# Performance work log

Hardware: AMD Instinct MI355X
Metric: run time of the kernel (lower is better)

Reference implementation:

```python
import jax, jax.numpy as jnp
import numpy as np

D_MODEL = 1024
N_HEADS = 16
D_FF = 4096
LN_EPS = 1e-5


def _layernorm(x, g, b):
    mu = jnp.mean(x, axis=-1, keepdims=True)
    var = jnp.var(x, axis=-1, keepdims=True)
    return (x - mu) * jax.lax.rsqrt(var + LN_EPS) * g + b


def setup_inputs() -> dict:
    key = jax.random.key(0)
    ks = jax.random.split(key, 10)
    N, B, C, F = 2048, 4, D_MODEL, D_FF
    s = lambda fan_in: 1.0 / np.sqrt(fan_in)
    return {
        "src": jax.random.normal(ks[0], (N, B, C), dtype=jnp.float32),
        "ln_g": jnp.ones((C,), jnp.float32),
        "ln_b": jnp.zeros((C,), jnp.float32),
        "w_qkv": jax.random.normal(ks[1], (C, 3 * C), jnp.float32) * s(C),
        "w_proj": jax.random.normal(ks[2], (C, C), jnp.float32) * s(C),
        "b_proj": jnp.zeros((C,), jnp.float32),
        "w1": jax.random.normal(ks[3], (C, F), jnp.float32) * s(C),
        "b1": jnp.zeros((F,), jnp.float32),
        "w2": jax.random.normal(ks[4], (F, C), jnp.float32) * s(F),
        "b2": jnp.zeros((C,), jnp.float32),
    }


def reference(src, ln_g, ln_b, w_qkv, w_proj, b_proj, w1, b1, w2, b2):
    N, B, C = src.shape
    H = N_HEADS
    hd = C // H
    scale = hd ** -0.5

    # pre-norm (norm_first=True)
    x = _layernorm(src, ln_g, ln_b)

    # qkv: (N,B,3C) -> (N,B,3,H,hd) -> permute(2,1,3,0,4) = (3,B,H,N,hd)
    qkv = (x @ w_qkv).reshape(N, B, 3, H, hd).transpose(2, 1, 3, 0, 4)
    q, k, v = qkv[0], qkv[1], qkv[2]  # (B,H,N,hd)

    attn = jax.nn.softmax(jnp.einsum("bhnd,bhmd->bhnm", q, k) * scale, axis=-1)
    o = jnp.einsum("bhnm,bhmd->bhnd", attn, v)  # (B,H,N,hd)
    # faithful to original: transpose(0,2) -> (N,H,B,hd), then reshape (N,B,C)
    o = o.transpose(2, 1, 0, 3).reshape(N, B, C)
    o = o @ w_proj + b_proj

    src = src + o
    # post_norm is Identity (norm_first=True)
    h = jax.nn.gelu(src @ w1 + b1, approximate=False)
    src = src + (h @ w2 + b2)
    return src
```

## Files before the change

### kernel.cpp

```cpp
#include <hip/hip_runtime.h>
#include <math.h>

typedef unsigned short u16;
typedef __attribute__((ext_vector_type(4))) unsigned short u16x4;
typedef __attribute__((ext_vector_type(8))) short short8;
typedef __attribute__((ext_vector_type(4))) float f32x4;

__device__ __forceinline__ void gl_lds16(const void* g, void* s) {
  __builtin_amdgcn_global_load_lds((const __attribute__((address_space(1))) void*)g,
                                   (__attribute__((address_space(3))) void*)s, 16, 0, 0);
}

__device__ __forceinline__ u16 f2bf(float f) {
  union { float f; unsigned u; } a; a.f = f;
  unsigned r = a.u + 0x7fff + ((a.u >> 16) & 1);
  return (u16)(r >> 16);
}

__global__ __launch_bounds__(256) void ln_kernel(const float* __restrict__ src,
                                                 const float* __restrict__ g,
                                                 const float* __restrict__ b,
                                                 u16* __restrict__ out) {
  int row = blockIdx.x;
  int t = threadIdx.x;
  const float4* s4 = (const float4*)(src + (size_t)row * 1024);
  float4 x = s4[t];
  float s1 = x.x + x.y + x.z + x.w;
  float s2 = x.x * x.x + x.y * x.y + x.z * x.z + x.w * x.w;
  for (int m = 32; m; m >>= 1) { s1 += __shfl_xor(s1, m); s2 += __shfl_xor(s2, m); }
  __shared__ float red[8];
  int w = t >> 6, lane = t & 63;
  if (lane == 0) { red[w] = s1; red[4 + w] = s2; }
  __syncthreads();
  float tot  = red[0] + red[1] + red[2] + red[3];
  float tot2 = red[4] + red[5] + red[6] + red[7];
  float mean = tot * (1.0f / 1024.0f);
  float var  = tot2 * (1.0f / 1024.0f) - mean * mean;
  float rs = rsqrtf(var + 1e-5f);
  float4 gg = ((const float4*)g)[t];
  float4 bb = ((const float4*)b)[t];
  u16x4 o;
  o[0] = f2bf((x.x - mean) * rs * gg.x + bb.x);
  o[1] = f2bf((x.y - mean) * rs * gg.y + bb.y);
  o[2] = f2bf((x.z - mean) * rs * gg.z + bb.z);
  o[3] = f2bf((x.w - mean) * rs * gg.w + bb.w);
  ((u16x4*)(out + (size_t)row * 1024))[t] = o;
}

__global__ __launch_bounds__(256) void tcast_kernel(const float* __restrict__ in,
                                                    u16* __restrict__ out, int K, int N) {
  __shared__ float tt[64][65];
  int t = threadIdx.x;
  int n0 = blockIdx.x * 64, k0 = blockIdx.y * 64;
  #pragma unroll
  for (int s = 0; s < 4; ++s) {
    int idx = s * 256 + t;
    int r = idx >> 4, c4 = idx & 15;
    float4 v = *(const float4*)(in + (size_t)(k0 + r) * N + n0 + c4 * 4);
    tt[r][c4 * 4 + 0] = v.x; tt[r][c4 * 4 + 1] = v.y;
    tt[r][c4 * 4 + 2] = v.z; tt[r][c4 * 4 + 3] = v.w;
  }
  __syncthreads();
  #pragma unroll
  for (int s = 0; s < 4; ++s) {
    int idx = s * 256 + t;
    int nr = idx >> 4, kc = idx & 15;
    u16x4 o;
    o[0] = f2bf(tt[kc * 4 + 0][nr]);
    o[1] = f2bf(tt[kc * 4 + 1][nr]);
    o[2] = f2bf(tt[kc * 4 + 2][nr]);
    o[3] = f2bf(tt[kc * 4 + 3][nr]);
    *(u16x4*)(out + (size_t)(n0 + nr) * K + k0 + kc * 4) = o;
  }
}

template <int EPI>
__global__ __launch_bounds__(256, 2) void gemm_kernel(
    const u16* __restrict__ A, const u16* __restrict__ Bt,
    int M, int N, int K,
    const float* __restrict__ bias, const float* __restrict__ resid,
    float* __restrict__ outf, u16* __restrict__ outh,
    u16* __restrict__ qo, u16* __restrict__ ko, u16* __restrict__ vo) {
  __shared__ u16 lA[128 * 32];
  __shared__ u16 lB[128 * 32];
  int t = threadIdx.x, w = t >> 6, lane = t & 63;
  int bm = blockIdx.x, bn = blockIdx.y;
  int wm = (w >> 1) * 64, wn = (w & 1) * 64;
  int am = lane & 15, ag = lane >> 4;
  f32x4 acc[4][4];
  #pragma unroll
  for (int i = 0; i < 4; ++i)
    #pragma unroll
    for (int j = 0; j < 4; ++j)
      #pragma unroll
      for (int r = 0; r < 4; ++r) acc[i][j][r] = 0.f;

  const size_t rowA0 = (size_t)bm * 128, colB0 = (size_t)bn * 128;

  for (int k0 = 0; k0 < K; k0 += 32) {
    #pragma unroll
    for (int s = 0; s < 2; ++s) {
      int c = s * 256 + w * 64 + lane;
      int row = c >> 2, cc = c & 3;
      int scc = cc ^ ((row >> 1) & 3);
      gl_lds16(A  + (rowA0 + row) * K + k0 + scc * 8, (char*)lA + (size_t)(s * 256 + w * 64) * 16);
      gl_lds16(Bt + (colB0 + row) * K + k0 + scc * 8, (char*)lB + (size_t)(s * 256 + w * 64) * 16);
    }
    __syncthreads();
    short8 af[4], bfr[4];
    #pragma unroll
    for (int i = 0; i < 4; ++i) {
      int row = wm + i * 16 + am;
      int ch = ag ^ ((row >> 1) & 3);
      af[i] = *(const short8*)(lA + row * 32 + ch * 8);
    }
    #pragma unroll
    for (int j = 0; j < 4; ++j) {
      int row = wn + j * 16 + am;
      int ch = ag ^ ((row >> 1) & 3);
      bfr[j] = *(const short8*)(lB + row * 32 + ch * 8);
    }
    #pragma unroll
    for (int i = 0; i < 4; ++i)
      #pragma unroll
      for (int j = 0; j < 4; ++j)
        acc[i][j] = __builtin_amdgcn_mfma_f32_16x16x32_bf16(af[i], bfr[j], acc[i][j], 0, 0, 0);
    __syncthreads();
  }

  #pragma unroll
  for (int i = 0; i < 4; ++i) {
    #pragma unroll
    for (int j = 0; j < 4; ++j) {
      #pragma unroll
      for (int r = 0; r < 4; ++r) {
        int grow = (int)rowA0 + wm + i * 16 + ag * 4 + r;
        int gcol = (int)colB0 + wn + j * 16 + am;
        float v = acc[i][j][r];
        if (EPI == 0) {
          int which = gcol >> 10, hh = (gcol >> 6) & 15, d = gcol & 63;
          int n = grow >> 2, bb = grow & 3;
          size_t hoff = (size_t)(bb * 16 + hh);
          if (which == 0)      qo[(hoff * 2048 + n) * 64 + d] = f2bf(v);
          else if (which == 1) ko[(hoff * 2048 + n) * 64 + d] = f2bf(v);
          else                 vo[hoff * 64 * 2048 + (size_t)d * 2048 + n] = f2bf(v);
        } else if (EPI == 1) {
          size_t idx = (size_t)grow * 1024 + gcol;
          float y = resid[idx] + v + bias[gcol];
          outf[idx] = y;
          outh[idx] = f2bf(y);
        } else if (EPI == 2) {
          float x = v + bias[gcol];
          float ge = 0.5f * x * (1.0f + erff(x * 0.70710678118654752f));
          outh[(size_t)grow * 4096 + gcol] = f2bf(ge);
        } else {
          size_t idx = (size_t)grow * 1024 + gcol;
          outf[idx] = resid[idx] + v + bias[gcol];
        }
      }
    }
  }
}

__global__ __launch_bounds__(256, 2) void attn_kernel(const u16* __restrict__ Q,
                                                      const u16* __restrict__ Kt,
                                                      const u16* __restrict__ Vt,
                                                      u16* __restrict__ Omix) {
  __shared__ u16 Qs[64 * 64], Ks[64 * 64], Vs[64 * 64];
  __shared__ u16 Ps[4][16 * 72];
  int t = threadIdx.x, w = t >> 6, lane = t & 63;
  int qb = blockIdx.x, bh = blockIdx.y;
  int bb = bh >> 4, hh = bh & 15;
  const u16* qbase = Q  + ((size_t)bh * 2048 + (size_t)qb * 64) * 64;
  const u16* kbase = Kt + (size_t)bh * 2048 * 64;
  const u16* vbase = Vt + (size_t)bh * 64 * 2048;
  int am = lane & 15, ag = lane >> 4;

  #pragma unroll
  for (int s = 0; s < 2; ++s) {
    int c = (w * 2 + s) * 64 + lane;
    int row = c >> 3, cc = c & 7;
    int scc = cc ^ (row & 7);
    gl_lds16(qbase + row * 64 + scc * 8, (char*)Qs + (size_t)(w * 2 + s) * 64 * 16);
  }
  __syncthreads();
  short8 qf[2];
  #pragma unroll
  for (int hf = 0; hf < 2; ++hf) {
    int row = w * 16 + am;
    int ch = (hf * 4 + ag) ^ (row & 7);
    qf[hf] = *(const short8*)(Qs + row * 64 + ch * 8);
  }

  float m[4], l[4];
  f32x4 o[4];
  #pragma unroll
  for (int r = 0; r < 4; ++r) { m[r] = -3.0e38f; l[r] = 0.f; }
  #pragma unroll
  for (int j = 0; j < 4; ++j)
    #pragma unroll
    for (int r = 0; r < 4; ++r) o[j][r] = 0.f;

  for (int kt = 0; kt < 32; ++kt) {
    int n0 = kt * 64;
    #pragma unroll
    for (int s = 0; s < 2; ++s) {
      int c = (w * 2 + s) * 64 + lane;
      int row = c >> 3, cc = c & 7;
      int scc = cc ^ (row & 7);
      gl_lds16(kbase + (size_t)(n0 + row) * 64 + scc * 8, (char*)Ks + (size_t)(w * 2 + s) * 64 * 16);
      gl_lds16(vbase + (size_t)row * 2048 + n0 + scc * 8, (char*)Vs + (size_t)(w * 2 + s) * 64 * 16);
    }
    __syncthreads();

    f32x4 sacc[4];
    #pragma unroll
    for (int jf = 0; jf < 4; ++jf)
      #pragma unroll
      for (int r = 0; r < 4; ++r) sacc[jf][r] = 0.f;
    #pragma unroll
    for (int jf = 0; jf < 4; ++jf) {
      #pragma unroll
      for (int hf = 0; hf < 2; ++hf) {
        int row = jf * 16 + am;
        int ch = (hf * 4 + ag) ^ (row & 7);
        short8 kf = *(const short8*)(Ks + row * 64 + ch * 8);
        sacc[jf] = __builtin_amdgcn_mfma_f32_16x16x32_bf16(qf[hf], kf, sacc[jf], 0, 0, 0);
      }
    }

    float pv[4][4], alpha[4];
    #pragma unroll
    for (int r = 0; r < 4; ++r) {
      float mx = fmaxf(fmaxf(sacc[0][r], sacc[1][r]), fmaxf(sacc[2][r], sacc[3][r])) * 0.125f;
      for (int msk = 1; msk < 16; msk <<= 1) mx = fmaxf(mx, __shfl_xor(mx, msk));
      float mnew = fmaxf(m[r], mx);
      alpha[r] = __expf(m[r] - mnew);
      float rs = 0.f;
      #pragma unroll
      for (int jf = 0; jf < 4; ++jf) {
        float p = __expf(sacc[jf][r] * 0.125f - mnew);
        pv[jf][r] = p;
        rs += p;
      }
      for (int msk = 1; msk < 16; msk <<= 1) rs += __shfl_xor(rs, msk);
      l[r] = l[r] * alpha[r] + rs;
      m[r] = mnew;
    }
    #pragma unroll
    for (int jf = 0; jf < 4; ++jf)
      #pragma unroll
      for (int r = 0; r < 4; ++r) o[jf][r] *= alpha[r];

    u16* pw = Ps[w];
    #pragma unroll
    for (int jf = 0; jf < 4; ++jf)
      #pragma unroll
      for (int r = 0; r < 4; ++r)
        pw[(ag * 4 + r) * 72 + jf * 16 + am] = f2bf(pv[jf][r]);

    short8 pf[2];
    #pragma unroll
    for (int kc = 0; kc < 2; ++kc)
      pf[kc] = *(const short8*)(pw + am * 72 + kc * 32 + ag * 8);

    #pragma unroll
    for (int jf = 0; jf < 4; ++jf) {
      #pragma unroll
      for (int kc = 0; kc < 2; ++kc) {
        int row = jf * 16 + am;
        int ch = (kc * 4 + ag) ^ (row & 7);
        short8 vf = *(const short8*)(Vs + row * 64 + ch * 8);
        o[jf] = __builtin_amdgcn_mfma_f32_16x16x32_bf16(pf[kc], vf, o[jf], 0, 0, 0);
      }
    }
    __syncthreads();
  }

  #pragma unroll
  for (int jf = 0; jf < 4; ++jf) {
    #pragma unroll
    for (int r = 0; r < 4; ++r) {
      int qrow = qb * 64 + w * 16 + ag * 4 + r;
      int d = jf * 16 + am;
      float val = o[jf][r] / l[r];
      Omix[((size_t)qrow * 4 + (hh >> 2)) * 1024 + (hh & 3) * 256 + bb * 64 + d] = f2bf(val);
    }
  }
}

extern "C" void kernel_launch(void* const* d_in, const int* in_sizes, int n_in,
                              void* d_out, int out_size, void* d_ws, size_t ws_size,
                              hipStream_t stream) {
  const float* src    = (const float*)d_in[0];
  const float* ln_g   = (const float*)d_in[1];
  const float* ln_b   = (const float*)d_in[2];
  const float* w_qkv  = (const float*)d_in[3];
  const float* w_proj = (const float*)d_in[4];
  const float* b_proj = (const float*)d_in[5];
  const float* w1     = (const float*)d_in[6];
  const float* b1     = (const float*)d_in[7];
  const float* w2     = (const float*)d_in[8];
  const float* b2     = (const float*)d_in[9];

  char* ws = (char*)d_ws;
  u16* wqkvT  = (u16*)(ws + 0);
  u16* wprojT = (u16*)(ws + 6291456);
  u16* w1T    = (u16*)(ws + 8388608);
  u16* w2T    = (u16*)(ws + 16777216);
  u16* xln    = (u16*)(ws + 25165824);
  u16* Omix   = xln;
  u16* Qp     = (u16*)(ws + 41943040);
  u16* Kp     = (u16*)(ws + 58720256);
  u16* Vp     = (u16*)(ws + 75497472);
  u16* hbuf   = (u16*)(ws + 41943040);
  u16* ybf    = (u16*)(ws + 109051904);
  float* yf   = (float*)d_out;

  dim3 blk(256);
  tcast_kernel<<<dim3(48, 16), blk, 0, stream>>>(w_qkv, wqkvT, 1024, 3072);
  tcast_kernel<<<dim3(16, 16), blk, 0, stream>>>(w_proj, wprojT, 1024, 1024);
  tcast_kernel<<<dim3(64, 16), blk, 0, stream>>>(w1, w1T, 1024, 4096);
  tcast_kernel<<<dim3(16, 64), blk, 0, stream>>>(w2, w2T, 4096, 1024);
  ln_kernel<<<8192, blk, 0, stream>>>(src, ln_g, ln_b, xln);

  gemm_kernel<0><<<dim3(64, 24), blk, 0, stream>>>(xln, wqkvT, 8192, 3072, 1024,
      nullptr, nullptr, nullptr, nullptr, Qp, Kp, Vp);

  attn_kernel<<<dim3(32, 64), blk, 0, stream>>>(Qp, Kp, Vp, Omix);

  gemm_kernel<1><<<dim3(64, 8), blk, 0, stream>>>(Omix, wprojT, 8192, 1024, 1024,
      b_proj, src, yf, ybf, nullptr, nullptr, nullptr);

  gemm_kernel<2><<<dim3(64, 32), blk, 0, stream>>>(ybf, w1T, 8192, 4096, 1024,
      b1, nullptr, nullptr, hbuf, nullptr, nullptr, nullptr);

  gemm_kernel<3><<<dim3(64, 8), blk, 0, stream>>>(hbuf, w2T, 8192, 1024, 4096,
      b2, yf, (float*)d_out, nullptr, nullptr, nullptr, nullptr);
}
```

Baseline: 639.9 us.

## Rewrite attention with 32x32 MFMA, double-buffered K/V, lazy rescale, separate V transpose

Attention is restructured so each block handles 256 queries (64 per wave) using 32x32x16 bf16 MFMAs. K^T Q is computed so probabilities stay in registers and feed the PV MFMA without an LDS round trip. K/V tiles are double-buffered via global_load_lds. The softmax uses exp2 with the scale folded into Q and skips rescaling when the running max grows by less than a threshold. The QKV GEMM now writes a plain row-major buffer, and a new kernel transposes V with a permuted key order matching the MFMA output layout. This removes scattered epilogue stores and per-tile P shuffles, at the cost of an extra kernel and more register pressure.

```diff
diff --git a/kernel.cpp b/kernel.cpp
--- a/kernel.cpp
+++ b/kernel.cpp
@@ -1,10 +1,12 @@
 #include <hip/hip_runtime.h>
+#include <hip/hip_bf16.h>
 #include <math.h>
 
 typedef unsigned short u16;
 typedef __attribute__((ext_vector_type(4))) unsigned short u16x4;
 typedef __attribute__((ext_vector_type(8))) short short8;
 typedef __attribute__((ext_vector_type(4))) float f32x4;
+typedef __attribute__((ext_vector_type(16))) float f32x16;
 
 __device__ __forceinline__ void gl_lds16(const void* g, void* s) {
   __builtin_amdgcn_global_load_lds((const __attribute__((address_space(1))) void*)g,
@@ -15,6 +17,34 @@
   union { float f; unsigned u; } a; a.f = f;
   unsigned r = a.u + 0x7fff + ((a.u >> 16) & 1);
   return (u16)(r >> 16);
+}
+
+__device__ __forceinline__ unsigned pk2(float a, float b) {
+  union { __hip_bfloat162 h; unsigned u; } cv;
+  cv.h = __float22bfloat162_rn(make_float2(a, b));
+  return cv.u;
+}
+
+__device__ __forceinline__ short8 mk8(unsigned a, unsigned b, unsigned c, unsigned d) {
+  union { unsigned u[4]; short8 v; } cv;
+  cv.u[0] = a; cv.u[1] = b; cv.u[2] = c; cv.u[3] = d; return cv.v;
+}
+
+__device__ __forceinline__ short8 scale8(short8 v, float s) {
+  short8 r;
+  #pragma unroll
+  for (int i = 0; i < 8; ++i) {
+    union { float f; unsigned u; } a; a.u = ((unsigned)(u16)v[i]) << 16;
+    r[i] = (short)f2bf(a.f * s);
+  }
+  return r;
+}
+
+__device__ __forceinline__ f32x16 z16() {
+  f32x16 z;
+  #pragma unroll
+  for (int i = 0; i < 16; ++i) z[i] = 0.f;
+  return z;
 }
 
 __global__ __launch_bounds__(256) void ln_kernel(const float* __restrict__ src,
@@ -74,13 +104,46 @@
   }
 }
 
+__global__ __launch_bounds__(256) void vtrans_kernel(const u16* __restrict__ qkv,
+                                                     u16* __restrict__ vt) {
+  __shared__ u16 tile[64][66];
+  int t = threadIdx.x;
+  int nt = blockIdx.x, bh = blockIdx.y;
+  int bb = bh >> 4, hh = bh & 15;
+  int n0 = nt * 64;
+  #pragma unroll
+  for (int s = 0; s < 2; ++s) {
+    int idx = s * 256 + t;
+    int i = idx >> 3, c = idx & 7;
+    union { short8 v; unsigned u[4]; } cv;
+    cv.v = *(const short8*)(qkv + (size_t)((n0 + i) * 4 + bb) * 3072 + 2048 + hh * 64 + c * 8);
+    unsigned* dst = (unsigned*)&tile[i][c * 8];
+    dst[0] = cv.u[0]; dst[1] = cv.u[1]; dst[2] = cv.u[2]; dst[3] = cv.u[3];
+  }
+  __syncthreads();
+  #pragma unroll
+  for (int s = 0; s < 2; ++s) {
+    int idx = s * 256 + t;
+    int d = idx >> 3, ch = idx & 7;
+    union { u16 e[8]; short8 v; } ov;
+    #pragma unroll
+    for (int j = 0; j < 8; ++j) {
+      int P = ch * 8 + j;
+      int q = P & 15, blk = q >> 2;
+      int bp = ((blk & 1) << 1) | (blk >> 1);
+      int src = (P & ~15) | (bp << 2) | (q & 3);
+      ov.e[j] = tile[src][d];
+    }
+    *(short8*)(vt + ((size_t)(bh * 64 + d)) * 2048 + n0 + ch * 8) = ov.v;
+  }
+}
+
 template <int EPI>
 __global__ __launch_bounds__(256, 2) void gemm_kernel(
     const u16* __restrict__ A, const u16* __restrict__ Bt,
     int M, int N, int K,
     const float* __restrict__ bias, const float* __restrict__ resid,
-    float* __restrict__ outf, u16* __restrict__ outh,
-    u16* __restrict__ qo, u16* __restrict__ ko, u16* __restrict__ vo) {
+    float* __restrict__ outf, u16* __restrict__ outh, int ldo) {
   __shared__ u16 lA[128 * 32];
   __shared__ u16 lB[128 * 32];
   int t = threadIdx.x, w = t >> 6, lane = t & 63;
@@ -138,12 +201,7 @@
         int gcol = (int)colB0 + wn + j * 16 + am;
         float v = acc[i][j][r];
         if (EPI == 0) {
-          int which = gcol >> 10, hh = (gcol >> 6) & 15, d = gcol & 63;
-          int n = grow >> 2, bb = grow & 3;
-          size_t hoff = (size_t)(bb * 16 + hh);
-          if (which == 0)      qo[(hoff * 2048 + n) * 64 + d] = f2bf(v);
-          else if (which == 1) ko[(hoff * 2048 + n) * 64 + d] = f2bf(v);
-          else                 vo[hoff * 64 * 2048 + (size_t)d * 2048 + n] = f2bf(v);
+          outh[(size_t)grow * ldo + gcol] = f2bf(v);
         } else if (EPI == 1) {
           size_t idx = (size_t)grow * 1024 + gcol;
           float y = resid[idx] + v + bias[gcol];
@@ -152,7 +210,7 @@
         } else if (EPI == 2) {
           float x = v + bias[gcol];
           float ge = 0.5f * x * (1.0f + erff(x * 0.70710678118654752f));
-          outh[(size_t)grow * 4096 + gcol] = f2bf(ge);
+          outh[(size_t)grow * ldo + gcol] = f2bf(ge);
         } else {
           size_t idx = (size_t)grow * 1024 + gcol;
           outf[idx] = resid[idx] + v + bias[gcol];
@@ -162,129 +220,132 @@
   }
 }
 
-__global__ __launch_bounds__(256, 2) void attn_kernel(const u16* __restrict__ Q,
-                                                      const u16* __restrict__ Kt,
-                                                      const u16* __restrict__ Vt,
-                                                      u16* __restrict__ Omix) {
-  __shared__ u16 Qs[64 * 64], Ks[64 * 64], Vs[64 * 64];
-  __shared__ u16 Ps[4][16 * 72];
-  int t = threadIdx.x, w = t >> 6, lane = t & 63;
-  int qb = blockIdx.x, bh = blockIdx.y;
-  int bb = bh >> 4, hh = bh & 15;
-  const u16* qbase = Q  + ((size_t)bh * 2048 + (size_t)qb * 64) * 64;
-  const u16* kbase = Kt + (size_t)bh * 2048 * 64;
-  const u16* vbase = Vt + (size_t)bh * 64 * 2048;
-  int am = lane & 15, ag = lane >> 4;
-
-  #pragma unroll
-  for (int s = 0; s < 2; ++s) {
-    int c = (w * 2 + s) * 64 + lane;
-    int row = c >> 3, cc = c & 7;
-    int scc = cc ^ (row & 7);
-    gl_lds16(qbase + row * 64 + scc * 8, (char*)Qs + (size_t)(w * 2 + s) * 64 * 16);
-  }
+#define SOFTMAX(S0, S1, MM, LL, OA, OB, WDS) { \
+  float smax = S0[0]; \
+  _Pragma("unroll") for (int i = 1; i < 16; ++i) smax = fmaxf(smax, S0[i]); \
+  _Pragma("unroll") for (int i = 0; i < 16; ++i) smax = fmaxf(smax, S1[i]); \
+  smax = fmaxf(smax, __shfl_xor(smax, 32)); \
+  if (!__all(smax <= MM + 11.5416f)) { \
+    float mn = fmaxf(MM, smax); float al = exp2f(MM - mn); \
+    LL *= al; \
+    _Pragma("unroll") for (int i = 0; i < 16; ++i) { OA[i] *= al; OB[i] *= al; } \
+    MM = mn; \
+  } \
+  float rsum = 0.f; \
+  _Pragma("unroll") for (int j = 0; j < 8; ++j) { \
+    float ea = exp2f(S0[2*j] - MM), eb = exp2f(S0[2*j+1] - MM); \
+    rsum += ea + eb; WDS[j] = pk2(ea, eb); } \
+  _Pragma("unroll") for (int j = 0; j < 8; ++j) { \
+    float ea = exp2f(S1[2*j] - MM), eb = exp2f(S1[2*j+1] - MM); \
+    rsum += ea + eb; WDS[8+j] = pk2(ea, eb); } \
+  rsum += __shfl_xor(rsum, 32); \
+  LL += rsum; }
+
+__global__ __launch_bounds__(256) void attn_kernel(const u16* __restrict__ qkv,
+                                                   const u16* __restrict__ Vt,
+                                                   u16* __restrict__ Omix) {
+  __shared__ u16 Ks[2][64 * 64];
+  __shared__ u16 Vs[2][64 * 64];
+  const int t = threadIdx.x, w = t >> 6, lane = t & 63, l31 = lane & 31, hi = lane >> 5;
+  const int qb = blockIdx.x, bh = blockIdx.y, bb = bh >> 4, hh = bh & 15;
+  const float SC = 0.125f * 1.44269504f;
+
+  short8 qf[2][4];
+  #pragma unroll
+  for (int qt = 0; qt < 2; ++qt)
+    #pragma unroll
+    for (int kc = 0; kc < 4; ++kc) {
+      int qn = qb * 256 + w * 64 + qt * 32 + l31;
+      const u16* p = qkv + (size_t)(qn * 4 + bb) * 3072 + hh * 64 + kc * 16 + hi * 8;
+      qf[qt][kc] = scale8(*(const short8*)p, SC);
+    }
+
+  float m0 = -1e30f, l0 = 0.f, m1 = -1e30f, l1 = 0.f;
+  f32x16 o00 = z16(), o01 = z16(), o10 = z16(), o11 = z16();
+
+#define STAGE(BUF, KT) { \
+  int n0_ = (KT) * 64; \
+  _Pragma("unroll") \
+  for (int s2 = 0; s2 < 2; ++s2) { \
+    int idx = s2 * 256 + t; \
+    int row = idx >> 3, c = idx & 7, sc = c ^ (row & 7); \
+    gl_lds16(qkv + (size_t)((n0_ + row) * 4 + bb) * 3072 + 1024 + hh * 64 + sc * 8, \
+             (char*)&Ks[BUF][0] + (s2 * 256 + w * 64) * 16); \
+    gl_lds16(Vt + ((size_t)(bh * 64 + row)) * 2048 + n0_ + sc * 8, \
+             (char*)&Vs[BUF][0] + (s2 * 256 + w * 64) * 16); \
+  } }
+
+  int cur = 0;
+  STAGE(0, 0);
   __syncthreads();
-  short8 qf[2];
-  #pragma unroll
-  for (int hf = 0; hf < 2; ++hf) {
-    int row = w * 16 + am;
-    int ch = (hf * 4 + ag) ^ (row & 7);
-    qf[hf] = *(const short8*)(Qs + row * 64 + ch * 8);
-  }
-
-  float m[4], l[4];
-  f32x4 o[4];
-  #pragma unroll
-  for (int r = 0; r < 4; ++r) { m[r] = -3.0e38f; l[r] = 0.f; }
-  #pragma unroll
-  for (int j = 0; j < 4; ++j)
-    #pragma unroll
-    for (int r = 0; r < 4; ++r) o[j][r] = 0.f;
 
   for (int kt = 0; kt < 32; ++kt) {
-    int n0 = kt * 64;
-    #pragma unroll
-    for (int s = 0; s < 2; ++s) {
-      int c = (w * 2 + s) * 64 + lane;
-      int row = c >> 3, cc = c & 7;
-      int scc = cc ^ (row & 7);
-      gl_lds16(kbase + (size_t)(n0 + row) * 64 + scc * 8, (char*)Ks + (size_t)(w * 2 + s) * 64 * 16);
-      gl_lds16(vbase + (size_t)row * 2048 + n0 + scc * 8, (char*)Vs + (size_t)(w * 2 + s) * 64 * 16);
-    }
+    if (kt < 31) STAGE(cur ^ 1, kt + 1);
+    const char* Kb = (const char*)&Ks[cur][0];
+    const char* Vb = (const char*)&Vs[cur][0];
+
+    short8 kf0[4], kf1[4];
+    #pragma unroll
+    for (int kc = 0; kc < 4; ++kc) {
+      int r0 = l31, r1 = 32 + l31;
+      kf0[kc] = *(const short8*)(Kb + r0 * 128 + (((kc * 2 + hi) ^ (r0 & 7)) * 16));
+      kf1[kc] = *(const short8*)(Kb + r1 * 128 + (((kc * 2 + hi) ^ (r1 & 7)) * 16));
+    }
+
+    f32x16 sA = z16(), sB = z16();
+    #pragma unroll
+    for (int kc = 0; kc < 4; ++kc) {
+      sA = __builtin_amdgcn_mfma_f32_32x32x16_bf16(kf0[kc], qf[0][kc], sA, 0, 0, 0);
+      sB = __builtin_amdgcn_mfma_f32_32x32x16_bf16(kf1[kc], qf[0][kc], sB, 0, 0, 0);
+    }
+    unsigned wd0[16];
+    SOFTMAX(sA, sB, m0, l0, o00, o01, wd0);
+
+    f32x16 sC = z16(), sD = z16();
+    #pragma unroll
+    for (int kc = 0; kc < 4; ++kc) {
+      sC = __builtin_amdgcn_mfma_f32_32x32x16_bf16(kf0[kc], qf[1][kc], sC, 0, 0, 0);
+      sD = __builtin_amdgcn_mfma_f32_32x32x16_bf16(kf1[kc], qf[1][kc], sD, 0, 0, 0);
+    }
+    unsigned wd1[16];
+    SOFTMAX(sC, sD, m1, l1, o10, o11, wd1);
+
+    short8 vf0[4], vf1[4];
+    #pragma unroll
+    for (int st = 0; st < 4; ++st) {
+      int r0 = l31, r1 = 32 + l31;
+      vf0[st] = *(const short8*)(Vb + r0 * 128 + (((st * 2 + hi) ^ (r0 & 7)) * 16));
+      vf1[st] = *(const short8*)(Vb + r1 * 128 + (((st * 2 + hi) ^ (r1 & 7)) * 16));
+    }
+
+    #pragma unroll
+    for (int st = 0; st < 4; ++st) {
+      short8 bA = mk8(wd0[4 * st], wd0[4 * st + 1], wd0[4 * st + 2], wd0[4 * st + 3]);
+      o00 = __builtin_amdgcn_mfma_f32_32x32x16_bf16(vf0[st], bA, o00, 0, 0, 0);
+      o01 = __builtin_amdgcn_mfma_f32_32x32x16_bf16(vf1[st], bA, o01, 0, 0, 0);
+      short8 bB = mk8(wd1[4 * st], wd1[4 * st + 1], wd1[4 * st + 2], wd1[4 * st + 3]);
+      o10 = __builtin_amdgcn_mfma_f32_32x32x16_bf16(vf0[st], bB, o10, 0, 0, 0);
+      o11 = __builtin_amdgcn_mfma_f32_32x32x16_bf16(vf1[st], bB, o11, 0, 0, 0);
+    }
+
     __syncthreads();
-
-    f32x4 sacc[4];
-    #pragma unroll
-    for (int jf = 0; jf < 4; ++jf)
+    cur ^= 1;
+  }
+
+  float r0 = 1.f / l0, r1 = 1.f / l1;
+  #pragma unroll
+  for (int qt = 0; qt < 2; ++qt) {
+    float rl = qt ? r1 : r0;
+    int qn = qb * 256 + w * 64 + qt * 32 + l31;
+    size_t base = ((size_t)(qn * 4 + (hh >> 2))) * 1024 + (hh & 3) * 256 + bb * 64;
+    #pragma unroll
+    for (int dt = 0; dt < 2; ++dt) {
       #pragma unroll
-      for (int r = 0; r < 4; ++r) sacc[jf][r] = 0.f;
-    #pragma unroll
-    for (int jf = 0; jf < 4; ++jf) {
-      #pragma unroll
-      for (int hf = 0; hf < 2; ++hf) {
-        int row = jf * 16 + am;
-        int ch = (hf * 4 + ag) ^ (row & 7);
-        short8 kf = *(const short8*)(Ks + row * 64 + ch * 8);
-        sacc[jf] = __builtin_amdgcn_mfma_f32_16x16x32_bf16(qf[hf], kf, sacc[jf], 0, 0, 0);
+      for (int reg = 0; reg < 16; ++reg) {
+        int d = dt * 32 + (reg & 3) + 8 * (reg >> 2) + 4 * hi;
+        float val = (qt ? (dt ? o11[reg] : o10[reg]) : (dt ? o01[reg] : o00[reg])) * rl;
+        Omix[base + d] = f2bf(val);
       }
-    }
-
-    float pv[4][4], alpha[4];
-    #pragma unroll
-    for (int r = 0; r < 4; ++r) {
-      float mx = fmaxf(fmaxf(sacc[0][r], sacc[1][r]), fmaxf(sacc[2][r], sacc[3][r])) * 0.125f;
-      for (int msk = 1; msk < 16; msk <<= 1) mx = fmaxf(mx, __shfl_xor(mx, msk));
-      float mnew = fmaxf(m[r], mx);
-      alpha[r] = __expf(m[r] - mnew);
-      float rs = 0.f;
-      #pragma unroll
-      for (int jf = 0; jf < 4; ++jf) {
-        float p = __expf(sacc[jf][r] * 0.125f - mnew);
-        pv[jf][r] = p;
-        rs += p;
-      }
-      for (int msk = 1; msk < 16; msk <<= 1) rs += __shfl_xor(rs, msk);
-      l[r] = l[r] * alpha[r] + rs;
-      m[r] = mnew;
-    }
-    #pragma unroll
-    for (int jf = 0; jf < 4; ++jf)
-      #pragma unroll
-      for (int r = 0; r < 4; ++r) o[jf][r] *= alpha[r];
-
-    u16* pw = Ps[w];
-    #pragma unroll
-    for (int jf = 0; jf < 4; ++jf)
-      #pragma unroll
-      for (int r = 0; r < 4; ++r)
-        pw[(ag * 4 + r) * 72 + jf * 16 + am] = f2bf(pv[jf][r]);
-
-    short8 pf[2];
-    #pragma unroll
-    for (int kc = 0; kc < 2; ++kc)
-      pf[kc] = *(const short8*)(pw + am * 72 + kc * 32 + ag * 8);
-
-    #pragma unroll
-    for (int jf = 0; jf < 4; ++jf) {
-      #pragma unroll
-      for (int kc = 0; kc < 2; ++kc) {
-        int row = jf * 16 + am;
-        int ch = (kc * 4 + ag) ^ (row & 7);
-        short8 vf = *(const short8*)(Vs + row * 64 + ch * 8);
-        o[jf] = __builtin_amdgcn_mfma_f32_16x16x32_bf16(pf[kc], vf, o[jf], 0, 0, 0);
-      }
-    }
-    __syncthreads();
-  }
-
-  #pragma unroll
-  for (int jf = 0; jf < 4; ++jf) {
-    #pragma unroll
-    for (int r = 0; r < 4; ++r) {
-      int qrow = qb * 64 + w * 16 + ag * 4 + r;
-      int d = jf * 16 + am;
-      float val = o[jf][r] / l[r];
-      Omix[((size_t)qrow * 4 + (hh >> 2)) * 1024 + (hh & 3) * 256 + bb * 64 + d] = f2bf(val);
     }
   }
 }
@@ -298,8 +359,8 @@
   const float* w_qkv  = (const float*)d_in[3];
   const float* w_proj = (const float*)d_in[4];
   const float* b_proj = (const float*)d_in[5];
+  const float* b1     = (const float*)d_in[7];
   const float* w1     = (const float*)d_in[6];
-  const float* b1     = (const float*)d_in[7];
   const float* w2     = (const float*)d_in[8];
   const float* b2     = (const float*)d_in[9];
 
@@ -310,9 +371,8 @@
   u16* w2T    = (u16*)(ws + 16777216);
   u16* xln    = (u16*)(ws + 25165824);
   u16* Omix   = xln;
-  u16* Qp     = (u16*)(ws + 41943040);
-  u16* Kp     = (u16*)(ws + 58720256);
-  u16* Vp     = (u16*)(ws + 75497472);
+  u16* qkv    = (u16*)(ws + 41943040);
+  u16* Vtb    = (u16*)(ws + 92274688);
   u16* hbuf   = (u16*)(ws + 41943040);
   u16* ybf    = (u16*)(ws + 109051904);
   float* yf   = (float*)d_out;
@@ -325,16 +385,18 @@
   ln_kernel<<<8192, blk, 0, stream>>>(src, ln_g, ln_b, xln);
 
   gemm_kernel<0><<<dim3(64, 24), blk, 0, stream>>>(xln, wqkvT, 8192, 3072, 1024,
-      nullptr, nullptr, nullptr, nullptr, Qp, Kp, Vp);
-
-  attn_kernel<<<dim3(32, 64), blk, 0, stream>>>(Qp, Kp, Vp, Omix);
+      nullptr, nullptr, nullptr, qkv, 3072);
+
+  vtrans_kernel<<<dim3(32, 64), blk, 0, stream>>>(qkv, Vtb);
+
+  attn_kernel<<<dim3(8, 64), blk, 0, stream>>>(qkv, Vtb, Omix);
 
   gemm_kernel<1><<<dim3(64, 8), blk, 0, stream>>>(Omix, wprojT, 8192, 1024, 1024,
-      b_proj, src, yf, ybf, nullptr, nullptr, nullptr);
+      b_proj, src, yf, ybf, 1024);
 
   gemm_kernel<2><<<dim3(64, 32), blk, 0, stream>>>(ybf, w1T, 8192, 4096, 1024,
-      b1, nullptr, nullptr, hbuf, nullptr, nullptr, nullptr);
+      b1, nullptr, nullptr, hbuf, 4096);
 
   gemm_kernel<3><<<dim3(64, 8), blk, 0, stream>>>(hbuf, w2T, 8192, 1024, 4096,
-      b2, yf, (float*)d_out, nullptr, nullptr, nullptr, nullptr);
-}
+      b2, yf, (float*)d_out, nullptr, 1024);
+}
```

New measurement: 593.9 us. -7.2%, faster.
